# Performance work log

Hardware: AMD Instinct MI355X
Metric: run time of the kernel (lower is better)

The kernel has to match this reference:

```python
import jax, jax.numpy as jnp
import numpy as np

B, T, S, H = 4, 128, 512, 512
LN_EPS = 1e-5


def setup_inputs() -> dict:
    key = jax.random.key(0)
    ks = jax.random.split(key, 10)
    query = jax.random.normal(ks[0], (B, T, H), dtype=jnp.float32)
    encoder_outputs = jax.random.normal(ks[1], (B, S, H), dtype=jnp.float32)
    src_lengths = jax.random.randint(ks[2], (B,), 1, S + 1, dtype=jnp.int32)
    # Parameters (nn.Linear stores weight as (out, in); we apply x @ W.T)
    W_h = jax.random.normal(ks[3], (H, H), dtype=jnp.float32) / np.sqrt(H)
    W_s = jax.random.normal(ks[4], (H, H), dtype=jnp.float32) / np.sqrt(H)
    v = jax.random.normal(ks[5], (H,), dtype=jnp.float32) * 0.01
    W_out = jax.random.normal(ks[6], (H, 2 * H), dtype=jnp.float32) / np.sqrt(2 * H)
    b_out = jnp.zeros((H,), dtype=jnp.float32)
    gamma = jnp.ones((H,), dtype=jnp.float32)
    beta = jnp.zeros((H,), dtype=jnp.float32)
    return {
        "query": query, "encoder_outputs": encoder_outputs, "src_lengths": src_lengths,
        "W_h": W_h, "W_s": W_s, "v": v, "W_out": W_out, "b_out": b_out,
        "gamma": gamma, "beta": beta,
    }


def reference(query, encoder_outputs, src_lengths, W_h, W_s, v, W_out, b_out, gamma, beta):
    # Project query and encoder states: (b,t,h) and (b,s,h)
    q_proj = jnp.einsum('bth,oh->bto', query, W_s)
    k_proj = jnp.einsum('bsh,oh->bso', encoder_outputs, W_h)
    # Additive score: tanh over broadcast-add, then dot with v -> (b,t,s)
    score = jnp.einsum('btsh,h->bts', jnp.tanh(q_proj[:, :, None, :] + k_proj[:, None, :, :]), v)
    # Mask padded source positions (src_idx >= length)
    pad = jnp.arange(S)[None, :] >= src_lengths[:, None]          # (b,s)
    score = jnp.where(pad[:, None, :], -jnp.inf, score)
    attn = jax.nn.softmax(score, axis=-1)                          # (b,t,s)
    context = jnp.einsum('bts,bsh->bth', attn, encoder_outputs)    # (b,t,h)
    cq = jnp.concatenate([context, query], axis=-1)                # (b,t,2h)
    out = jnp.tanh(jnp.einsum('btk,ok->bto', cq, W_out) + b_out)
    # LayerNorm over last dim
    mu = jnp.mean(out, axis=-1, keepdims=True)
    var = jnp.mean(jnp.square(out - mu), axis=-1, keepdims=True)
    return (out - mu) / jnp.sqrt(var + LN_EPS) * gamma + beta
```

## Files before the change

kernel.cpp:

```cpp
#include <hip/hip_runtime.h>
#include <hip/hip_bf16.h>
#include <math.h>

#define B 4
#define T 128
#define S 512
#define H 512
#define QK_SCALE 2.8853900817779268f

#if defined(__has_builtin)
#if __has_builtin(__builtin_amdgcn_exp2f)
#define EXP2F(x) __builtin_amdgcn_exp2f(x)
#else
#define EXP2F(x) __expf((x) * 0.6931471805599453f)
#endif
#else
#define EXP2F(x) __expf((x) * 0.6931471805599453f)
#endif

typedef __attribute__((ext_vector_type(8))) short bf16x8;
typedef __attribute__((ext_vector_type(4))) float f32x4;

__device__ __forceinline__ short f2b(float x) {
    unsigned int u = __float_as_uint(x);
    u += 0x7fffu + ((u >> 16) & 1u);
    return (short)(u >> 16);
}
__device__ __forceinline__ float fast_tanh(float x) {
    float e = __expf(2.0f * x);
    float r = __builtin_amdgcn_rcpf(e + 1.0f);
    return 1.0f - 2.0f * r;
}

__global__ __launch_bounds__(256) void cvt_all(
    const float* __restrict__ q, const float* __restrict__ Ws,
    const float* __restrict__ Wh, const float* __restrict__ Wo,
    const float* __restrict__ enc,
    short* __restrict__ qb, short* __restrict__ wsb, short* __restrict__ whb,
    short* __restrict__ wob, short* __restrict__ eb) {
    size_t i = ((size_t)blockIdx.x * 256 + threadIdx.x) * 8;
    const float* src; short* dst; size_t off;
    if (i < 262144)        { src = q;   dst = qb;  off = i; }
    else if (i < 524288)   { src = Ws;  dst = wsb; off = i - 262144; }
    else if (i < 786432)   { src = Wh;  dst = whb; off = i - 524288; }
    else if (i < 1310720)  { src = Wo;  dst = wob; off = i - 786432; }
    else                   { src = enc; dst = eb;  off = i - 1310720; }
    float4 a = *(const float4*)(src + off);
    float4 b = *(const float4*)(src + off + 4);
    ushort4 o0 = make_ushort4((unsigned short)f2b(a.x), (unsigned short)f2b(a.y),
                              (unsigned short)f2b(a.z), (unsigned short)f2b(a.w));
    ushort4 o1 = make_ushort4((unsigned short)f2b(b.x), (unsigned short)f2b(b.y),
                              (unsigned short)f2b(b.z), (unsigned short)f2b(b.w));
    *(ushort4*)(dst + off) = o0;
    *(ushort4*)(dst + off + 4) = o1;
}

__global__ __launch_bounds__(64) void proj_mega(
    const short* __restrict__ qb, const short* __restrict__ eb,
    const short* __restrict__ wsb, const short* __restrict__ whb,
    const short* __restrict__ wob, const int* __restrict__ slen,
    float* __restrict__ qe, float* __restrict__ ke,
    short* __restrict__ ewt, float* __restrict__ qw) {
    const int job = blockIdx.x;
    const int lane = threadIdx.x;
    const int r = lane & 15, kb = lane >> 4;
    const short* A; int lda;
    const short* W; int ldw;
    int epi;
    float* Cf = nullptr; short* Cb = nullptr; int ldc;
    if (job < 256) {
        const int m0 = (job >> 4) * 32, n0 = (job & 15) * 32;
        A = qb + (size_t)m0 * H; lda = H;
        W = wsb + (size_t)n0 * H; ldw = H;
        Cf = qe + (size_t)m0 * H + n0; ldc = H; epi = 0;
    } else if (job < 1280) {
        const int j = job - 256;
        const int m0 = (j >> 4) * 32, n0 = (j & 15) * 32;
        if ((m0 & 511) >= slen[m0 >> 9]) return;
        A = eb + (size_t)m0 * H; lda = H;
        W = whb + (size_t)n0 * H; ldw = H;
        Cf = ke + (size_t)m0 * H + n0; ldc = H; epi = 0;
    } else if (job < 2304) {
        const int j = job - 1280;
        const int b = j >> 8;
        const int m0 = ((j >> 4) & 15) * 32;
        const int n0 = (j & 15) * 32;
        if (n0 >= slen[b]) return;
        A = wob + (size_t)m0 * (2 * H); lda = 2 * H;
        W = eb + ((size_t)b * S + n0) * H; ldw = H;
        Cb = ewt + (size_t)b * H * S + (size_t)m0 * S + n0; ldc = S; epi = 1;
    } else {
        const int j = job - 2304;
        const int m0 = (j >> 4) * 32, n0 = (j & 15) * 32;
        A = qb + (size_t)m0 * H; lda = H;
        W = wob + (size_t)n0 * (2 * H) + H; ldw = 2 * H;
        Cf = qw + (size_t)m0 * H + n0; ldc = H; epi = 2;
    }
    const short* a0p = A + (size_t)r * lda + kb * 8;
    const short* a1p = a0p + (size_t)16 * lda;
    const short* b0p = W + (size_t)r * ldw + kb * 8;
    const short* b1p = b0p + (size_t)16 * ldw;
    f32x4 acc00 = {0,0,0,0}, acc01 = {0,0,0,0}, acc10 = {0,0,0,0}, acc11 = {0,0,0,0};
#pragma unroll 4
    for (int k = 0; k < H; k += 32) {
        bf16x8 a0 = *(const bf16x8*)(a0p + k);
        bf16x8 a1 = *(const bf16x8*)(a1p + k);
        bf16x8 b0 = *(const bf16x8*)(b0p + k);
        bf16x8 b1 = *(const bf16x8*)(b1p + k);
        acc00 = __builtin_amdgcn_mfma_f32_16x16x32_bf16(a0, b0, acc00, 0, 0, 0);
        acc01 = __builtin_amdgcn_mfma_f32_16x16x32_bf16(a0, b1, acc01, 0, 0, 0);
        acc10 = __builtin_amdgcn_mfma_f32_16x16x32_bf16(a1, b0, acc10, 0, 0, 0);
        acc11 = __builtin_amdgcn_mfma_f32_16x16x32_bf16(a1, b1, acc11, 0, 0, 0);
    }
    const int cr = kb * 4, cc = r;
    if (epi == 0) {
#pragma unroll
        for (int g = 0; g < 4; ++g) {
            Cf[(size_t)(cr + g) * ldc + cc]           = EXP2F(acc00[g] * QK_SCALE);
            Cf[(size_t)(cr + g) * ldc + 16 + cc]      = EXP2F(acc01[g] * QK_SCALE);
            Cf[(size_t)(16 + cr + g) * ldc + cc]      = EXP2F(acc10[g] * QK_SCALE);
            Cf[(size_t)(16 + cr + g) * ldc + 16 + cc] = EXP2F(acc11[g] * QK_SCALE);
        }
    } else if (epi == 1) {
#pragma unroll
        for (int g = 0; g < 4; ++g) {
            Cb[(size_t)(cr + g) * ldc + cc]           = f2b(acc00[g]);
            Cb[(size_t)(cr + g) * ldc + 16 + cc]      = f2b(acc01[g]);
            Cb[(size_t)(16 + cr + g) * ldc + cc]      = f2b(acc10[g]);
            Cb[(size_t)(16 + cr + g) * ldc + 16 + cc] = f2b(acc11[g]);
        }
    } else {
#pragma unroll
        for (int g = 0; g < 4; ++g) {
            Cf[(size_t)(cr + g) * ldc + cc]           = acc00[g];
            Cf[(size_t)(cr + g) * ldc + 16 + cc]      = acc01[g];
            Cf[(size_t)(16 + cr + g) * ldc + cc]      = acc10[g];
            Cf[(size_t)(16 + cr + g) * ldc + 16 + cc] = acc11[g];
        }
    }
}

__global__ __launch_bounds__(64) void score_v6(
    const float* __restrict__ qe, const float* __restrict__ ke,
    const float* __restrict__ v, const int* __restrict__ slen,
    float* __restrict__ scoreh) {
    const int qt = blockIdx.z & 3;
    const int b = blockIdx.z >> 2;
    const int L = slen[b];
    const int sbase = blockIdx.x * 64;
    if (sbase >= L) return;
    const int t0 = blockIdx.y * 4;
    const int hbase = qt * 128;
    __shared__ __align__(16) float qs[4][132];
    __shared__ __align__(16) float vsh[132];
    const int lane = threadIdx.x;
    {
        const int tr = lane >> 4, c = (lane & 15) * 8;
        const float* qsrc = qe + (size_t)(b * T + t0 + tr) * H + hbase + c;
        *(float4*)&qs[tr][c]     = *(const float4*)qsrc;
        *(float4*)&qs[tr][c + 4] = *(const float4*)(qsrc + 4);
        if (lane < 32) {
            float4 vv = *(const float4*)&v[hbase + lane * 4];
            *(float4*)&vsh[lane * 4] =
                make_float4(-2.f * vv.x, -2.f * vv.y, -2.f * vv.z, -2.f * vv.w);
        }
    }
    __syncthreads();
    const float* krow = ke + (size_t)(b * S + sbase + lane) * H + hbase;
    float acc0 = 0.f, acc1 = 0.f, acc2 = 0.f, acc3 = 0.f;
#pragma unroll
    for (int chunk = 0; chunk < 2; ++chunk) {
        const int ho = chunk * 64;
        float4 kv[16];
#pragma unroll
        for (int j = 0; j < 16; ++j)
            kv[j] = *(const float4*)(krow + ho + j * 4);
#pragma unroll
        for (int j = 0; j < 16; ++j) {
            float4 v4 = *(const float4*)&vsh[ho + j * 4];
            float4 q0 = *(const float4*)&qs[0][ho + j * 4];
            float4 q1 = *(const float4*)&qs[1][ho + j * 4];
            float4 q2 = *(const float4*)&qs[2][ho + j * 4];
            float4 q3 = *(const float4*)&qs[3][ho + j * 4];
            acc0 = fmaf(v4.x, __builtin_amdgcn_rcpf(fmaf(q0.x, kv[j].x, 1.f)), acc0);
            acc1 = fmaf(v4.x, __builtin_amdgcn_rcpf(fmaf(q1.x, kv[j].x, 1.f)), acc1);
            acc2 = fmaf(v4.x, __builtin_amdgcn_rcpf(fmaf(q2.x, kv[j].x, 1.f)), acc2);
            acc3 = fmaf(v4.x, __builtin_amdgcn_rcpf(fmaf(q3.x, kv[j].x, 1.f)), acc3);
            acc0 = fmaf(v4.y, __builtin_amdgcn_rcpf(fmaf(q0.y, kv[j].y, 1.f)), acc0);
            acc1 = fmaf(v4.y, __builtin_amdgcn_rcpf(fmaf(q1.y, kv[j].y, 1.f)), acc1);
            acc2 = fmaf(v4.y, __builtin_amdgcn_rcpf(fmaf(q2.y, kv[j].y, 1.f)), acc2);
            acc3 = fmaf(v4.y, __builtin_amdgcn_rcpf(fmaf(q3.y, kv[j].y, 1.f)), acc3);
            acc0 = fmaf(v4.z, __builtin_amdgcn_rcpf(fmaf(q0.z, kv[j].z, 1.f)), acc0);
            acc1 = fmaf(v4.z, __builtin_amdgcn_rcpf(fmaf(q1.z, kv[j].z, 1.f)), acc1);
            acc2 = fmaf(v4.z, __builtin_amdgcn_rcpf(fmaf(q2.z, kv[j].z, 1.f)), acc2);
            acc3 = fmaf(v4.z, __builtin_amdgcn_rcpf(fmaf(q3.z, kv[j].z, 1.f)), acc3);
            acc0 = fmaf(v4.w, __builtin_amdgcn_rcpf(fmaf(q0.w, kv[j].w, 1.f)), acc0);
            acc1 = fmaf(v4.w, __builtin_amdgcn_rcpf(fmaf(q1.w, kv[j].w, 1.f)), acc1);
            acc2 = fmaf(v4.w, __builtin_amdgcn_rcpf(fmaf(q2.w, kv[j].w, 1.f)), acc2);
            acc3 = fmaf(v4.w, __builtin_amdgcn_rcpf(fmaf(q3.w, kv[j].w, 1.f)), acc3);
        }
    }
    const size_t obase = ((size_t)qt * (B * T) + b * T + t0) * S + sbase + lane;
    scoreh[obase]         = acc0;
    scoreh[obase + S]     = acc1;
    scoreh[obase + 2 * S] = acc2;
    scoreh[obase + 3 * S] = acc3;
}

__global__ __launch_bounds__(256) void combine_k(
    const float* __restrict__ scoreh, const int* __restrict__ slen,
    short* __restrict__ U, float* __restrict__ Z) {
    const int row = blockIdx.x * 4 + (threadIdx.x >> 6);
    const int lane = threadIdx.x & 63;
    const int L = slen[row >> 7];
    const size_t sl = (size_t)(B * T) * S;
    const float* p = scoreh + (size_t)row * S + lane * 8;
    float e[8];
    float sm = 0.f;
#pragma unroll
    for (int j = 0; j < 2; ++j) {
        float4 q0 = *(const float4*)(p + j * 4);
        float4 q1 = *(const float4*)(p + sl + j * 4);
        float4 q2 = *(const float4*)(p + 2 * sl + j * 4);
        float4 q3 = *(const float4*)(p + 3 * sl + j * 4);
        e[j * 4 + 0] = __expf(q0.x + q1.x + q2.x + q3.x);
        e[j * 4 + 1] = __expf(q0.y + q1.y + q2.y + q3.y);
        e[j * 4 + 2] = __expf(q0.z + q1.z + q2.z + q3.z);
        e[j * 4 + 3] = __expf(q0.w + q1.w + q2.w + q3.w);
    }
    const int cbase = lane * 8;
#pragma unroll
    for (int j = 0; j < 8; ++j) {
        if (cbase + j >= L) e[j] = 0.f;
        sm += e[j];
    }
#pragma unroll
    for (int off = 1; off < 64; off <<= 1) sm += __shfl_xor(sm, off);
    if (lane == 0) Z[row] = sm;
    short* o = U + (size_t)row * S + cbase;
    ushort4 u0 = make_ushort4((unsigned short)f2b(e[0]), (unsigned short)f2b(e[1]),
                              (unsigned short)f2b(e[2]), (unsigned short)f2b(e[3]));
    ushort4 u1 = make_ushort4((unsigned short)f2b(e[4]), (unsigned short)f2b(e[5]),
                              (unsigned short)f2b(e[6]), (unsigned short)f2b(e[7]));
    *(ushort4*)o = u0;
    *(ushort4*)(o + 4) = u1;
}

__global__ __launch_bounds__(64) void mfma_out2(
    const short* __restrict__ U, const short* __restrict__ ewt,
    const float* __restrict__ qw, const float* __restrict__ Z,
    const int* __restrict__ slen, const float* __restrict__ bias,
    float* __restrict__ pre) {
    const int lane = threadIdx.x;
    const int r = lane & 15, kb = lane >> 4;
    const int m0 = blockIdx.y * 32;
    const int n0 = blockIdx.x * 32;
    const int b = m0 >> 7;
    const int L = slen[b];
    const int Keff = min(S, (L + 31) & ~31);
    const short* A = U + (size_t)m0 * S;
    const short* Bp = ewt + (size_t)b * H * S;
    const short* a0p = A + (size_t)r * S + kb * 8;
    const short* a1p = a0p + 16 * S;
    const short* b0p = Bp + (size_t)(n0 + r) * S + kb * 8;
    const short* b1p = b0p + 16 * S;
    f32x4 acc00 = {0,0,0,0}, acc01 = {0,0,0,0}, acc10 = {0,0,0,0}, acc11 = {0,0,0,0};
#pragma unroll 2
    for (int k = 0; k < Keff; k += 32) {
        bf16x8 a0 = *(const bf16x8*)(a0p + k);
        bf16x8 a1 = *(const bf16x8*)(a1p + k);
        bf16x8 b0 = *(const bf16x8*)(b0p + k);
        bf16x8 b1 = *(const bf16x8*)(b1p + k);
        acc00 = __builtin_amdgcn_mfma_f32_16x16x32_bf16(a0, b0, acc00, 0, 0, 0);
        acc01 = __builtin_amdgcn_mfma_f32_16x16x32_bf16(a0, b1, acc01, 0, 0, 0);
        acc10 = __builtin_amdgcn_mfma_f32_16x16x32_bf16(a1, b0, acc10, 0, 0, 0);
        acc11 = __builtin_amdgcn_mfma_f32_16x16x32_bf16(a1, b1, acc11, 0, 0, 0);
    }
    const int cr = kb * 4, cc = r;
    float bn0 = bias[n0 + cc], bn1 = bias[n0 + 16 + cc];
#pragma unroll
    for (int g = 0; g < 4; ++g) {
        const int gr0 = m0 + cr + g;
        const int gr1 = gr0 + 16;
        float iz0 = __builtin_amdgcn_rcpf(Z[gr0]);
        float iz1 = __builtin_amdgcn_rcpf(Z[gr1]);
        size_t row0 = (size_t)gr0 * H;
        size_t row1 = (size_t)gr1 * H;
        pre[row0 + n0 + cc]      = fast_tanh(fmaf(acc00[g], iz0, qw[row0 + n0 + cc]) + bn0);
        pre[row0 + n0 + 16 + cc] = fast_tanh(fmaf(acc01[g], iz0, qw[row0 + n0 + 16 + cc]) + bn1);
        pre[row1 + n0 + cc]      = fast_tanh(fmaf(acc10[g], iz1, qw[row1 + n0 + cc]) + bn0);
        pre[row1 + n0 + 16 + cc] = fast_tanh(fmaf(acc11[g], iz1, qw[row1 + n0 + 16 + cc]) + bn1);
    }
}

__global__ __launch_bounds__(256) void ln_out(
    const float* __restrict__ X, const float* __restrict__ gamma,
    const float* __restrict__ beta, float* __restrict__ out) {
    __shared__ float red[8];
    const int r = blockIdx.x;
    const int tid = threadIdx.x;
    const int lane = tid & 63, wv = tid >> 6;
    const float* x = X + (size_t)r * H;
    float x0 = x[tid], x1 = x[tid + 256];
    float s = x0 + x1;
#pragma unroll
    for (int off = 32; off > 0; off >>= 1) s += __shfl_down(s, off);
    if (lane == 0) red[wv] = s;
    __syncthreads();
    float mu = (red[0] + red[1] + red[2] + red[3]) * (1.0f / H);
    float d0 = x0 - mu, d1 = x1 - mu;
    float vsum = d0 * d0 + d1 * d1;
#pragma unroll
    for (int off = 32; off > 0; off >>= 1) vsum += __shfl_down(vsum, off);
    if (lane == 0) red[4 + wv] = vsum;
    __syncthreads();
    float var = (red[4] + red[5] + red[6] + red[7]) * (1.0f / H);
    float inv = rsqrtf(var + 1e-5f);
    out[(size_t)r * H + tid] = d0 * inv * gamma[tid] + beta[tid];
    out[(size_t)r * H + tid + 256] = d1 * inv * gamma[tid + 256] + beta[tid + 256];
}

extern "C" void kernel_launch(void* const* d_in, const int* in_sizes, int n_in,
                              void* d_out, int out_size, void* d_ws, size_t ws_size,
                              hipStream_t stream) {
    const float* query = (const float*)d_in[0];
    const float* enc   = (const float*)d_in[1];
    const int*   slen  = (const int*)d_in[2];
    const float* W_h   = (const float*)d_in[3];
    const float* W_s   = (const float*)d_in[4];
    const float* v     = (const float*)d_in[5];
    const float* W_out = (const float*)d_in[6];
    const float* b_out = (const float*)d_in[7];
    const float* gamma = (const float*)d_in[8];
    const float* beta  = (const float*)d_in[9];
    float* out = (float*)d_out;

    char* base = (char*)d_ws;
    short* qb     = (short*)(base + 0x000000);
    short* wsb    = (short*)(base + 0x080000);
    short* whb    = (short*)(base + 0x100000);
    short* wob    = (short*)(base + 0x180000);
    short* eb     = (short*)(base + 0x280000);
    float* qe     = (float*)(base + 0x480000);
    float* ke     = (float*)(base + 0x580000);
    float* scoreh = (float*)(base + 0x980000);
    short* U      = (short*)(base + 0xD80000);
    short* ewt    = (short*)(base + 0xE00000);
    float* qw     = (float*)(base + 0x1000000);
    float* Z      = (float*)(base + 0x1100000);
    float* pre    = (float*)(base + 0x1101000);

    cvt_all<<<dim3(1152), dim3(256), 0, stream>>>(query, W_s, W_h, W_out, enc,
                                                  qb, wsb, whb, wob, eb);
    proj_mega<<<dim3(2560), dim3(64), 0, stream>>>(qb, eb, wsb, whb, wob, slen,
                                                   qe, ke, ewt, qw);
    score_v6<<<dim3(8, 32, 16), dim3(64), 0, stream>>>(qe, ke, v, slen, scoreh);
    combine_k<<<dim3(128), dim3(256), 0, stream>>>(scoreh, slen, U, Z);
    mfma_out2<<<dim3(16, 16), dim3(64), 0, stream>>>(U, ewt, qw, Z, slen, b_out, pre);
    ln_out<<<dim3(B * T), dim3(256), 0, stream>>>(pre, gamma, beta, out);
}
```

Baseline: 71.05 us.

## Store exp-transformed key projection transposed so score kernel reads coalesced columns

The key projection epilogue now writes exp2-scaled values into an (b,h,s) transposed buffer with float4 stores. The score kernel then reads one scalar per h per lane from this buffer, so adjacent lanes (adjacent s) load contiguous addresses instead of each lane streaming its own 512-float row. This replaces the strided per-lane float4 loads and the large register arrays. The cost is scalar LDS broadcast reads per h and more load instructions in the inner loop.

```diff
diff --git a/kernel.cpp b/kernel.cpp
--- a/kernel.cpp
+++ b/kernel.cpp
@@ -59,7 +59,7 @@
     const short* __restrict__ qb, const short* __restrict__ eb,
     const short* __restrict__ wsb, const short* __restrict__ whb,
     const short* __restrict__ wob, const int* __restrict__ slen,
-    float* __restrict__ qe, float* __restrict__ ke,
+    float* __restrict__ qe, float* __restrict__ keT,
     short* __restrict__ ewt, float* __restrict__ qw) {
     const int job = blockIdx.x;
     const int lane = threadIdx.x;
@@ -68,6 +68,7 @@
     const short* W; int ldw;
     int epi;
     float* Cf = nullptr; short* Cb = nullptr; int ldc;
+    int bT = 0, m0T = 0, n0T = 0;
     if (job < 256) {
         const int m0 = (job >> 4) * 32, n0 = (job & 15) * 32;
         A = qb + (size_t)m0 * H; lda = H;
@@ -79,7 +80,7 @@
         if ((m0 & 511) >= slen[m0 >> 9]) return;
         A = eb + (size_t)m0 * H; lda = H;
         W = whb + (size_t)n0 * H; ldw = H;
-        Cf = ke + (size_t)m0 * H + n0; ldc = H; epi = 0;
+        epi = 3; bT = m0 >> 9; m0T = m0 & 511; n0T = n0;
     } else if (job < 2304) {
         const int j = job - 1280;
         const int b = j >> 8;
@@ -113,7 +114,21 @@
         acc11 = __builtin_amdgcn_mfma_f32_16x16x32_bf16(a1, b1, acc11, 0, 0, 0);
     }
     const int cr = kb * 4, cc = r;
-    if (epi == 0) {
+    if (epi == 3) {
+        float* base = keT + ((size_t)bT * H + n0T + cc) * S + m0T + cr;
+        float4 w00 = make_float4(EXP2F(acc00[0] * QK_SCALE), EXP2F(acc00[1] * QK_SCALE),
+                                 EXP2F(acc00[2] * QK_SCALE), EXP2F(acc00[3] * QK_SCALE));
+        float4 w01 = make_float4(EXP2F(acc01[0] * QK_SCALE), EXP2F(acc01[1] * QK_SCALE),
+                                 EXP2F(acc01[2] * QK_SCALE), EXP2F(acc01[3] * QK_SCALE));
+        float4 w10 = make_float4(EXP2F(acc10[0] * QK_SCALE), EXP2F(acc10[1] * QK_SCALE),
+                                 EXP2F(acc10[2] * QK_SCALE), EXP2F(acc10[3] * QK_SCALE));
+        float4 w11 = make_float4(EXP2F(acc11[0] * QK_SCALE), EXP2F(acc11[1] * QK_SCALE),
+                                 EXP2F(acc11[2] * QK_SCALE), EXP2F(acc11[3] * QK_SCALE));
+        *(float4*)base              = w00;
+        *(float4*)(base + 16 * S)   = w01;
+        *(float4*)(base + 16)       = w10;
+        *(float4*)(base + 16 * S + 16) = w11;
+    } else if (epi == 0) {
 #pragma unroll
         for (int g = 0; g < 4; ++g) {
             Cf[(size_t)(cr + g) * ldc + cc]           = EXP2F(acc00[g] * QK_SCALE);
@@ -140,8 +155,8 @@
     }
 }
 
-__global__ __launch_bounds__(64) void score_v6(
-    const float* __restrict__ qe, const float* __restrict__ ke,
+__global__ __launch_bounds__(64) void score_v7(
+    const float* __restrict__ qe, const float* __restrict__ keT,
     const float* __restrict__ v, const int* __restrict__ slen,
     float* __restrict__ scoreh) {
     const int qt = blockIdx.z & 3;
@@ -152,7 +167,7 @@
     const int t0 = blockIdx.y * 4;
     const int hbase = qt * 128;
     __shared__ __align__(16) float qs[4][132];
-    __shared__ __align__(16) float vsh[132];
+    __shared__ __align__(16) float vsh[128];
     const int lane = threadIdx.x;
     {
         const int tr = lane >> 4, c = (lane & 15) * 8;
@@ -166,39 +181,17 @@
         }
     }
     __syncthreads();
-    const float* krow = ke + (size_t)(b * S + sbase + lane) * H + hbase;
+    const float* kcol = keT + ((size_t)b * H + hbase) * S + sbase + lane;
     float acc0 = 0.f, acc1 = 0.f, acc2 = 0.f, acc3 = 0.f;
-#pragma unroll
-    for (int chunk = 0; chunk < 2; ++chunk) {
-        const int ho = chunk * 64;
-        float4 kv[16];
-#pragma unroll
-        for (int j = 0; j < 16; ++j)
-            kv[j] = *(const float4*)(krow + ho + j * 4);
-#pragma unroll
-        for (int j = 0; j < 16; ++j) {
-            float4 v4 = *(const float4*)&vsh[ho + j * 4];
-            float4 q0 = *(const float4*)&qs[0][ho + j * 4];
-            float4 q1 = *(const float4*)&qs[1][ho + j * 4];
-            float4 q2 = *(const float4*)&qs[2][ho + j * 4];
-            float4 q3 = *(const float4*)&qs[3][ho + j * 4];
-            acc0 = fmaf(v4.x, __builtin_amdgcn_rcpf(fmaf(q0.x, kv[j].x, 1.f)), acc0);
-            acc1 = fmaf(v4.x, __builtin_amdgcn_rcpf(fmaf(q1.x, kv[j].x, 1.f)), acc1);
-            acc2 = fmaf(v4.x, __builtin_amdgcn_rcpf(fmaf(q2.x, kv[j].x, 1.f)), acc2);
-            acc3 = fmaf(v4.x, __builtin_amdgcn_rcpf(fmaf(q3.x, kv[j].x, 1.f)), acc3);
-            acc0 = fmaf(v4.y, __builtin_amdgcn_rcpf(fmaf(q0.y, kv[j].y, 1.f)), acc0);
-            acc1 = fmaf(v4.y, __builtin_amdgcn_rcpf(fmaf(q1.y, kv[j].y, 1.f)), acc1);
-            acc2 = fmaf(v4.y, __builtin_amdgcn_rcpf(fmaf(q2.y, kv[j].y, 1.f)), acc2);
-            acc3 = fmaf(v4.y, __builtin_amdgcn_rcpf(fmaf(q3.y, kv[j].y, 1.f)), acc3);
-            acc0 = fmaf(v4.z, __builtin_amdgcn_rcpf(fmaf(q0.z, kv[j].z, 1.f)), acc0);
-            acc1 = fmaf(v4.z, __builtin_amdgcn_rcpf(fmaf(q1.z, kv[j].z, 1.f)), acc1);
-            acc2 = fmaf(v4.z, __builtin_amdgcn_rcpf(fmaf(q2.z, kv[j].z, 1.f)), acc2);
-            acc3 = fmaf(v4.z, __builtin_amdgcn_rcpf(fmaf(q3.z, kv[j].z, 1.f)), acc3);
-            acc0 = fmaf(v4.w, __builtin_amdgcn_rcpf(fmaf(q0.w, kv[j].w, 1.f)), acc0);
-            acc1 = fmaf(v4.w, __builtin_amdgcn_rcpf(fmaf(q1.w, kv[j].w, 1.f)), acc1);
-            acc2 = fmaf(v4.w, __builtin_amdgcn_rcpf(fmaf(q2.w, kv[j].w, 1.f)), acc2);
-            acc3 = fmaf(v4.w, __builtin_amdgcn_rcpf(fmaf(q3.w, kv[j].w, 1.f)), acc3);
-        }
+#pragma unroll 8
+    for (int h = 0; h < 128; ++h) {
+        float kv = kcol[(size_t)h * S];
+        float vh = vsh[h];
+        float q0 = qs[0][h], q1 = qs[1][h], q2 = qs[2][h], q3 = qs[3][h];
+        acc0 = fmaf(vh, __builtin_amdgcn_rcpf(fmaf(q0, kv, 1.f)), acc0);
+        acc1 = fmaf(vh, __builtin_amdgcn_rcpf(fmaf(q1, kv, 1.f)), acc1);
+        acc2 = fmaf(vh, __builtin_amdgcn_rcpf(fmaf(q2, kv, 1.f)), acc2);
+        acc3 = fmaf(vh, __builtin_amdgcn_rcpf(fmaf(q3, kv, 1.f)), acc3);
     }
     const size_t obase = ((size_t)qt * (B * T) + b * T + t0) * S + sbase + lane;
     scoreh[obase]         = acc0;
@@ -342,7 +335,7 @@
     short* wob    = (short*)(base + 0x180000);
     short* eb     = (short*)(base + 0x280000);
     float* qe     = (float*)(base + 0x480000);
-    float* ke     = (float*)(base + 0x580000);
+    float* keT    = (float*)(base + 0x580000);
     float* scoreh = (float*)(base + 0x980000);
     short* U      = (short*)(base + 0xD80000);
     short* ewt    = (short*)(base + 0xE00000);
@@ -353,8 +346,8 @@
     cvt_all<<<dim3(1152), dim3(256), 0, stream>>>(query, W_s, W_h, W_out, enc,
                                                   qb, wsb, whb, wob, eb);
     proj_mega<<<dim3(2560), dim3(64), 0, stream>>>(qb, eb, wsb, whb, wob, slen,
-                                                   qe, ke, ewt, qw);
-    score_v6<<<dim3(8, 32, 16), dim3(64), 0, stream>>>(qe, ke, v, slen, scoreh);
+                                                   qe, keT, ewt, qw);
+    score_v7<<<dim3(8, 32, 16), dim3(64), 0, stream>>>(qe, keT, v, slen, scoreh);
     combine_k<<<dim3(128), dim3(256), 0, stream>>>(scoreh, slen, U, Z);
     mfma_out2<<<dim3(16, 16), dim3(64), 0, stream>>>(U, ewt, qw, Z, slen, b_out, pre);
     ln_out<<<dim3(B * T), dim3(256), 0, stream>>>(pre, gamma, beta, out);
```

Result: faster. 62.51 us (-12.0%).
